# Optimization experiments

Hardware: AMD Instinct MI355X
Metric: run time of the kernel (lower is better)

## Reference

```python
import jax, jax.numpy as jnp
import numpy as np

NUM_CLASSES = 19
FEAT_CH = 512
N = 524288  # B*H*W flattened pixels


def setup_inputs() -> dict:
    key = jax.random.key(0)
    k1, k2 = jax.random.split(key)
    features = jax.random.normal(k1, (N, FEAT_CH), dtype=jnp.float32)
    labels = jax.random.randint(k2, (N,), 0, 20, dtype=jnp.int64 if jax.config.jax_enable_x64 else jnp.int32)
    return {"features": features, "labels": labels, "ignore_label": 19}


def reference(features, labels, ignore_label):
    """Faithful, efficient version of get_centroid_vector.

    Original builds an (N, C, A) onehot-expanded tensor and sums over N.
    Mathematically this is a per-class segment sum of valid pixels:
      mean[c]       = sum_{i: lab_i==c, valid} feat_i / max(count_c, 1)
      sum_weight[c] = count_c broadcast over A
      class_dist[c] = count_c
    """
    C, A = NUM_CLASSES, features.shape[1]
    valid = labels != ignore_label
    w = valid.astype(features.dtype)                      # (N,)
    lab = jnp.where(valid, labels, 0).astype(jnp.int32)   # ignored -> bucket 0 w/ weight 0
    sums = jax.ops.segment_sum(features * w[:, None], lab, num_segments=C)  # (C, A)
    counts = jax.ops.segment_sum(w, lab, num_segments=C)                    # (C,)
    amount = jnp.where(counts == 0, jnp.ones_like(counts), counts)          # Amount_CXA[==0]=1
    mean = sums / amount[:, None]
    sum_weight = jnp.broadcast_to(counts[:, None], (C, A))
    class_dist = counts
    return mean, sum_weight, class_dist
```

## Files before the change

### kernel.cpp

```cpp
#include <hip/hip_runtime.h>

#define NUM_CLASSES 19
#define FEAT_CH 512
#define ACC_SLOTS (NUM_CLASSES * FEAT_CH)

constexpr int BLOCK = 512;
constexpr int NBLK  = 1024;

__global__ __launch_bounds__(BLOCK, 8)
void bars_accum_kernel(const float* __restrict__ feat,
                       const int* __restrict__ labels,
                       const int* __restrict__ ignore_p,
                       float* __restrict__ gsum,
                       float* __restrict__ gcnt,
                       int n) {
    __shared__ float ssum[ACC_SLOTS];
    __shared__ float scnt[NUM_CLASSES];

    const int tid = threadIdx.x;
    for (int s = tid; s < ACC_SLOTS; s += BLOCK) ssum[s] = 0.f;
    if (tid < NUM_CLASSES) scnt[tid] = 0.f;
    __syncthreads();

    const int ign = ignore_p[0];

    const int per_blk = (n + (int)gridDim.x - 1) / (int)gridDim.x;
    const int p_begin = (int)blockIdx.x * per_blk;
    const int p_end   = min(n, p_begin + per_blk);

    const int sub = tid >> 7;
    const int cg  = tid & 127;
    const float4* __restrict__ feat4 = (const float4*)feat;

    for (int p0 = p_begin; p0 < p_end; p0 += 4) {
        const int p = p0 + sub;
        if (p < p_end) {
            const int lab = labels[p];
            if (lab != ign) {
                const float4 v = feat4[(size_t)p * (FEAT_CH / 4) + cg];
                float* dst = &ssum[lab * FEAT_CH];
                atomicAdd(&dst[0 * 128 + cg], v.x);
                atomicAdd(&dst[1 * 128 + cg], v.y);
                atomicAdd(&dst[2 * 128 + cg], v.z);
                atomicAdd(&dst[3 * 128 + cg], v.w);
                if (cg == 0) atomicAdd(&scnt[lab], 1.0f);
            }
        }
    }
    __syncthreads();

    for (int g = tid; g < ACC_SLOTS; g += BLOCK) {
        const int c   = g >> 9;
        const int ch  = g & 511;
        const int j   = ch & 3;
        const int cgf = ch >> 2;
        const float v = ssum[c * FEAT_CH + j * 128 + cgf];
        if (v != 0.f) atomicAdd(&gsum[g], v);
    }
    if (tid < NUM_CLASSES) {
        const float c = scnt[tid];
        if (c != 0.f) atomicAdd(&gcnt[tid], c);
    }
}

__global__ void bars_finalize_kernel(const float* __restrict__ gsum,
                                     const float* __restrict__ gcnt,
                                     float* __restrict__ out) {
    const int i = blockIdx.x * blockDim.x + threadIdx.x;
    if (i < ACC_SLOTS) {
        const int c = i >> 9;
        const float cnt = gcnt[c];
        const float amt = (cnt == 0.f) ? 1.f : cnt;
        out[i] = gsum[i] / amt;
        out[ACC_SLOTS + i] = cnt;
    }
    if (i < NUM_CLASSES) {
        out[2 * ACC_SLOTS + i] = gcnt[i];
    }
}

extern "C" void kernel_launch(void* const* d_in, const int* in_sizes, int n_in,
                              void* d_out, int out_size, void* d_ws, size_t ws_size,
                              hipStream_t stream) {
    const float* feat   = (const float*)d_in[0];
    const int*   labels = (const int*)d_in[1];
    const int*   ign    = (const int*)d_in[2];
    float*       out    = (float*)d_out;

    const int n = in_sizes[1];

    float* gsum = (float*)d_ws;
    float* gcnt = gsum + ACC_SLOTS;

    hipMemsetAsync(d_ws, 0, (ACC_SLOTS + NUM_CLASSES) * sizeof(float), stream);
    bars_accum_kernel<<<NBLK, BLOCK, 0, stream>>>(feat, labels, ign, gsum, gcnt, n);
    bars_finalize_kernel<<<(ACC_SLOTS + 255) / 256, 256, 0, stream>>>(gsum, gcnt, out);
}
```

Baseline: 2.362 ms.

## Replace global atomic reduction with per-block partial slabs and separate reduce kernel

Each block now writes its shared-memory class sums to a private workspace slab, falling back to atomics into K shared slabs when the workspace is too small. A new reduce kernel then sums the slabs per output element and divides by the counts. The main loop also handles two pixels per iteration with branch-free masking and clamped indices, so loads can be issued early. This removes contention from 1024 blocks issuing global atomics on the same 9.7K addresses, but adds writing and rereading up to about 40MB of partials. The masked path also performs shared atomics for ignored pixels.

Result: slower. 2.555 ms (+8.2%).

```diff
diff --git a/kernel.cpp b/kernel.cpp
--- a/kernel.cpp
+++ b/kernel.cpp
@@ -3,6 +3,7 @@
 #define NUM_CLASSES 19
 #define FEAT_CH 512
 #define ACC_SLOTS (NUM_CLASSES * FEAT_CH)
+#define CNT_STRIDE 32
 
 constexpr int BLOCK = 512;
 constexpr int NBLK  = 1024;
@@ -11,9 +12,9 @@
 void bars_accum_kernel(const float* __restrict__ feat,
                        const int* __restrict__ labels,
                        const int* __restrict__ ignore_p,
-                       float* __restrict__ gsum,
-                       float* __restrict__ gcnt,
-                       int n) {
+                       float* __restrict__ part,
+                       float* __restrict__ cnts,
+                       int n, int K) {
     __shared__ float ssum[ACC_SLOTS];
     __shared__ float scnt[NUM_CLASSES];
 
@@ -32,51 +33,90 @@
     const int cg  = tid & 127;
     const float4* __restrict__ feat4 = (const float4*)feat;
 
-    for (int p0 = p_begin; p0 < p_end; p0 += 4) {
-        const int p = p0 + sub;
-        if (p < p_end) {
-            const int lab = labels[p];
-            if (lab != ign) {
-                const float4 v = feat4[(size_t)p * (FEAT_CH / 4) + cg];
-                float* dst = &ssum[lab * FEAT_CH];
-                atomicAdd(&dst[0 * 128 + cg], v.x);
-                atomicAdd(&dst[1 * 128 + cg], v.y);
-                atomicAdd(&dst[2 * 128 + cg], v.z);
-                atomicAdd(&dst[3 * 128 + cg], v.w);
-                if (cg == 0) atomicAdd(&scnt[lab], 1.0f);
-            }
+    for (int p0 = p_begin; p0 < p_end; p0 += 8) {
+        const int pa  = p0 + sub;
+        const int pb  = p0 + 4 + sub;
+        const int pca = min(pa, p_end - 1);
+        const int pcb = min(pb, p_end - 1);
+        const int la  = labels[pca];
+        const int lb  = labels[pcb];
+        const float4 va = feat4[(size_t)pca * (FEAT_CH / 4) + cg];
+        const float4 vb = feat4[(size_t)pcb * (FEAT_CH / 4) + cg];
+        const float wa = (la != ign && pa < p_end) ? 1.f : 0.f;
+        const float wb = (lb != ign && pb < p_end) ? 1.f : 0.f;
+        const int   ca = (la != ign) ? la : 0;
+        const int   cb = (lb != ign) ? lb : 0;
+        float* da = &ssum[ca * FEAT_CH];
+        float* db = &ssum[cb * FEAT_CH];
+        atomicAdd(&da[0 * 128 + cg], va.x * wa);
+        atomicAdd(&da[1 * 128 + cg], va.y * wa);
+        atomicAdd(&da[2 * 128 + cg], va.z * wa);
+        atomicAdd(&da[3 * 128 + cg], va.w * wa);
+        atomicAdd(&db[0 * 128 + cg], vb.x * wb);
+        atomicAdd(&db[1 * 128 + cg], vb.y * wb);
+        atomicAdd(&db[2 * 128 + cg], vb.z * wb);
+        atomicAdd(&db[3 * 128 + cg], vb.w * wb);
+        if (cg == 0) {
+            atomicAdd(&scnt[ca], wa);
+            atomicAdd(&scnt[cb], wb);
         }
     }
     __syncthreads();
 
-    for (int g = tid; g < ACC_SLOTS; g += BLOCK) {
-        const int c   = g >> 9;
-        const int ch  = g & 511;
-        const int j   = ch & 3;
-        const int cgf = ch >> 2;
-        const float v = ssum[c * FEAT_CH + j * 128 + cgf];
-        if (v != 0.f) atomicAdd(&gsum[g], v);
-    }
-    if (tid < NUM_CLASSES) {
-        const float c = scnt[tid];
-        if (c != 0.f) atomicAdd(&gcnt[tid], c);
+    const int slab = (int)blockIdx.x % K;
+    float* __restrict__ ps = part + (size_t)slab * ACC_SLOTS;
+    if (K == (int)gridDim.x) {
+        for (int g = tid; g < ACC_SLOTS; g += BLOCK) {
+            const int c = g >> 9, ch = g & 511, j = ch & 3, cgf = ch >> 2;
+            ps[g] = ssum[c * FEAT_CH + j * 128 + cgf];
+        }
+        if (tid < NUM_CLASSES) cnts[(size_t)slab * CNT_STRIDE + tid] = scnt[tid];
+    } else {
+        for (int g = tid; g < ACC_SLOTS; g += BLOCK) {
+            const int c = g >> 9, ch = g & 511, j = ch & 3, cgf = ch >> 2;
+            const float v = ssum[c * FEAT_CH + j * 128 + cgf];
+            if (v != 0.f) atomicAdd(&ps[g], v);
+        }
+        if (tid < NUM_CLASSES) {
+            const float c = scnt[tid];
+            if (c != 0.f) atomicAdd(&cnts[(size_t)slab * CNT_STRIDE + tid], c);
+        }
     }
 }
 
-__global__ void bars_finalize_kernel(const float* __restrict__ gsum,
-                                     const float* __restrict__ gcnt,
-                                     float* __restrict__ out) {
-    const int i = blockIdx.x * blockDim.x + threadIdx.x;
-    if (i < ACC_SLOTS) {
-        const int c = i >> 9;
-        const float cnt = gcnt[c];
-        const float amt = (cnt == 0.f) ? 1.f : cnt;
-        out[i] = gsum[i] / amt;
-        out[ACC_SLOTS + i] = cnt;
+__global__ __launch_bounds__(256)
+void bars_reduce_kernel(const float* __restrict__ part,
+                        const float* __restrict__ cnts,
+                        float* __restrict__ out, int K) {
+    __shared__ float scnt[NUM_CLASSES];
+    const int tid = threadIdx.x;
+    if (tid < NUM_CLASSES) scnt[tid] = 0.f;
+    __syncthreads();
+
+    const int c = tid & (CNT_STRIDE - 1);
+    float cacc = 0.f;
+    for (int idx = tid; idx < K * CNT_STRIDE; idx += 256)
+        cacc += cnts[idx];
+    if (c < NUM_CLASSES) atomicAdd(&scnt[c], cacc);
+    __syncthreads();
+
+    const int g = (int)blockIdx.x * 256 + tid;
+    float a0 = 0.f, a1 = 0.f, a2 = 0.f, a3 = 0.f;
+    int k = 0;
+    for (; k + 4 <= K; k += 4) {
+        a0 += part[(size_t)(k + 0) * ACC_SLOTS + g];
+        a1 += part[(size_t)(k + 1) * ACC_SLOTS + g];
+        a2 += part[(size_t)(k + 2) * ACC_SLOTS + g];
+        a3 += part[(size_t)(k + 3) * ACC_SLOTS + g];
     }
-    if (i < NUM_CLASSES) {
-        out[2 * ACC_SLOTS + i] = gcnt[i];
-    }
+    for (; k < K; ++k) a0 += part[(size_t)k * ACC_SLOTS + g];
+    const float s   = (a0 + a1) + (a2 + a3);
+    const float cnt = scnt[g >> 9];
+    const float amt = (cnt == 0.f) ? 1.f : cnt;
+    out[g] = s / amt;
+    out[ACC_SLOTS + g] = cnt;
+    if (blockIdx.x == 0 && tid < NUM_CLASSES)
+        out[2 * ACC_SLOTS + tid] = scnt[tid];
 }
 
 extern "C" void kernel_launch(void* const* d_in, const int* in_sizes, int n_in,
@@ -89,10 +129,17 @@
 
     const int n = in_sizes[1];
 
-    float* gsum = (float*)d_ws;
-    float* gcnt = gsum + ACC_SLOTS;
+    const size_t slab_bytes = (size_t)(ACC_SLOTS + CNT_STRIDE) * sizeof(float);
+    int K = (int)(ws_size / slab_bytes);
+    if (K > NBLK) K = NBLK;
+    if (K < 1)    K = 1;
 
-    hipMemsetAsync(d_ws, 0, (ACC_SLOTS + NUM_CLASSES) * sizeof(float), stream);
-    bars_accum_kernel<<<NBLK, BLOCK, 0, stream>>>(feat, labels, ign, gsum, gcnt, n);
-    bars_finalize_kernel<<<(ACC_SLOTS + 255) / 256, 256, 0, stream>>>(gsum, gcnt, out);
+    float* part = (float*)d_ws;
+    float* cnts = part + (size_t)K * ACC_SLOTS;
+
+    if (K < NBLK) {
+        hipMemsetAsync(d_ws, 0, (size_t)K * slab_bytes, stream);
+    }
+    bars_accum_kernel<<<NBLK, BLOCK, 0, stream>>>(feat, labels, ign, part, cnts, n, K);
+    bars_reduce_kernel<<<ACC_SLOTS / 256, 256, 0, stream>>>(part, cnts, out, K);
 }
```
